# Performance work log

Measured on AMD Instinct MI355X. Metric: run time of the kernel, lower is better.

Reference implementation:

```python
import jax, jax.numpy as jnp
import numpy as np

B, N, D, H, W = 2, 6, 120, 32, 88
C = 128
Z, HO, WO = 1, 128, 128  # bev_feat_shape
N_POINTS = 1_000_000


def setup_inputs() -> dict:
    key = jax.random.key(0)
    k1, k2, k3, k4, k5 = jax.random.split(key, 5)
    depth = jax.random.normal(k1, (B, N, D, H, W), dtype=jnp.float32)
    feat = jax.random.normal(k2, (B, N, C, H, W), dtype=jnp.float32)
    ranks_depth = jax.random.randint(k3, (N_POINTS,), 0, B * N * D * H * W, dtype=jnp.int32)
    ranks_feat = jax.random.randint(k4, (N_POINTS,), 0, B * N * H * W, dtype=jnp.int32)
    ranks_bev = jnp.sort(jax.random.randint(k5, (N_POINTS,), 0, B * Z * HO * WO, dtype=jnp.int32))
    # Derive intervals (consecutive runs of equal ranks_bev), as the CUDA op expects.
    rb = np.asarray(ranks_bev)
    starts = np.concatenate([[0], np.nonzero(np.diff(rb))[0] + 1]).astype(np.int32)
    lengths = np.diff(np.concatenate([starts, [rb.shape[0]]])).astype(np.int32)
    return {
        "depth": depth,
        "feat": feat,
        "ranks_depth": ranks_depth,
        "ranks_feat": ranks_feat,
        "ranks_bev": ranks_bev,
        "interval_starts": jnp.asarray(starts),
        "interval_lengths": jnp.asarray(lengths),
    }


def reference(depth, feat, ranks_depth, ranks_feat, ranks_bev, interval_starts, interval_lengths):
    b, n, c, h, w = feat.shape
    # feat laid out [b,n,c,h,w]; ranks_feat indexes (b,n,h,w) positions -> put c last.
    feat_flat = feat.transpose(0, 1, 3, 4, 2).reshape(-1, c)  # [b*n*h*w, c]
    depth_flat = depth.reshape(-1)                            # [b*n*d*h*w]
    # Gather depth scalar and feature row per point, multiply.
    prod = depth_flat[ranks_depth][:, None] * feat_flat[ranks_feat]  # [n_points, c]
    # Interval-based accumulation == segment-sum over sorted ranks_bev.
    num_cells = b * Z * HO * WO
    out = jax.ops.segment_sum(prod, ranks_bev, num_segments=num_cells)  # [b*z*h*w, c]
    out = out.reshape(b, Z, HO, WO, c).transpose(0, 4, 1, 2, 3)  # [b, c, z, h, w]
    return out
```

## Files before the change

kernel.cpp:

```cpp
#include <hip/hip_runtime.h>
#include <hip/hip_bf16.h>

#define HW_    2816
#define C_     128
#define BN_    12
#define SPAT_  16384
#define CELLS_ 32768
#define CB_    64

#define TF_BX     88
#define TF_BY     4
#define TF_BLOCKS (TF_BX * TF_BY * BN_)
#define PG_BLOCKS 1024
#define IV_BLOCKS 128

__device__ __forceinline__ unsigned int f2bf_rne(float x) {
    const unsigned int u = __float_as_uint(x);
    return (u + 0x7fffu + ((u >> 16) & 1u)) >> 16;
}

__global__ __launch_bounds__(256) void prep_k(
        const float* __restrict__ feat, __hip_bfloat16* __restrict__ featT,
        const float* __restrict__ depth, const int* __restrict__ rd,
        const int* __restrict__ rf, unsigned int* __restrict__ pair, int n_points,
        const int* __restrict__ istart, const int* __restrict__ ilen,
        const int* __restrict__ rb, int4* __restrict__ iv4,
        int* __restrict__ map, int n_intervals) {
    __shared__ float tile[32][33];
    const int bid = blockIdx.x;
    const int tid = threadIdx.x;

    if (bid < TF_BLOCKS) {
        const int bn  = bid / (TF_BX * TF_BY);
        const int r   = bid - bn * (TF_BX * TF_BY);
        const int c0  = (r / TF_BX) * 32;
        const int hw0 = (r - (r / TF_BX) * TF_BX) * 32;
        const int x = tid & 31, y = tid >> 5;
        const float* src = feat + ((size_t)bn * C_ + c0) * HW_ + hw0;
        #pragma unroll
        for (int yy = y; yy < 32; yy += 8)
            tile[yy][x] = src[(size_t)yy * HW_ + x];
        __syncthreads();
        __hip_bfloat16* dst = featT + ((size_t)bn * HW_ + hw0) * C_ + c0;
        #pragma unroll
        for (int yy = y; yy < 32; yy += 8)
            dst[(size_t)yy * C_ + x] = __float2bfloat16(tile[x][yy]);
    } else if (bid < TF_BLOCKS + PG_BLOCKS) {
        const int t = (bid - TF_BLOCKS) * 256 + tid;
        const int stride = PG_BLOCKS * 256;
        for (int base = t; base < n_points; base += 4 * stride) {
            int ii[4], idx[4], rfv[4];
            float v[4];
            #pragma unroll
            for (int u = 0; u < 4; ++u) {
                ii[u] = base + u * stride;
                const int cl = ii[u] < n_points ? ii[u] : base;
                idx[u] = rd[cl];
                rfv[u] = rf[cl];
            }
            #pragma unroll
            for (int u = 0; u < 4; ++u) v[u] = depth[idx[u]];
            #pragma unroll
            for (int u = 0; u < 4; ++u)
                if (ii[u] < n_points)
                    pair[ii[u]] = (f2bf_rne(v[u]) << 16) | (unsigned)rfv[u];
        }
    } else {
        const int ivl = (bid - TF_BLOCKS - PG_BLOCKS) * 256 + tid;
        if (ivl < n_intervals) {
            const int s = istart[ivl];
            const int c = rb[s];
            iv4[ivl] = make_int4(s, ilen[ivl], c, 0);
            map[c] = ivl;
            const int cnext = (ivl + 1 < n_intervals) ? rb[istart[ivl + 1]] : CELLS_;
            for (int cc = c + 1; cc < cnext; ++cc) map[cc] = -1;
            if (ivl == 0) for (int cc = 0; cc < c; ++cc) map[cc] = -1;
        }
    }
}

__global__ __launch_bounds__(1024, 4) void bevpool_cells_k(
        const unsigned int* __restrict__ pair,
        const uint4* __restrict__ featT,
        const int4* __restrict__ iv4,
        const int* __restrict__ map,
        float* __restrict__ out) {
    __shared__ float lds[CB_][68];
    const int half  = blockIdx.x & 1;
    const int cb    = blockIdx.x >> 1;
    const int cell0 = cb * CB_;
    const int tid   = threadIdx.x;

    #pragma unroll
    for (int i = tid; i < CB_ * 68; i += 1024) (&lds[0][0])[i] = 0.f;
    __syncthreads();

    const int widx = tid >> 6;
    const int lane = tid & 63;
    const int grp  = lane >> 3;
    const int sl   = lane & 7;
    const size_t hoff = (size_t)(half * 8 + sl);
    const int cl0  = widx * 4;

    const int4 m4 = *(const int4*)&map[cell0 + cl0];
    const int m[4] = {m4.x, m4.y, m4.z, m4.w};
    int4 vq[4];
    #pragma unroll
    for (int q = 0; q < 4; ++q) vq[q] = iv4[m[q] < 0 ? 0 : m[q]];

    #pragma unroll
    for (int q = 0; q < 4; ++q) {
        if (m[q] < 0) continue;
        const int start = vq[q].x;
        const int end   = vq[q].x + vq[q].y;

        float acc[8] = {0.f, 0.f, 0.f, 0.f, 0.f, 0.f, 0.f, 0.f};
        for (int i = start + grp; i < end; i += 32) {
            int cl_[4];
            unsigned pr_[4];
            float d_[4];
            uint4 f_[4];
            #pragma unroll
            for (int u = 0; u < 4; ++u) {
                const int ii = i + 8 * u;
                cl_[u] = (ii < end) ? ii : i;
            }
            #pragma unroll
            for (int u = 0; u < 4; ++u) pr_[u] = pair[cl_[u]];
            #pragma unroll
            for (int u = 0; u < 4; ++u) d_[u] = __uint_as_float(pr_[u] & 0xffff0000u);
            #pragma unroll
            for (int u = 1; u < 4; ++u) d_[u] = (i + 8 * u < end) ? d_[u] : 0.f;
            #pragma unroll
            for (int u = 0; u < 4; ++u)
                f_[u] = featT[(size_t)(pr_[u] & 0xffffu) * 16 + hoff];
            #pragma unroll
            for (int u = 0; u < 4; ++u) {
                const float d = d_[u];
                acc[0] = fmaf(d, __uint_as_float(f_[u].x << 16),         acc[0]);
                acc[1] = fmaf(d, __uint_as_float(f_[u].x & 0xffff0000u), acc[1]);
                acc[2] = fmaf(d, __uint_as_float(f_[u].y << 16),         acc[2]);
                acc[3] = fmaf(d, __uint_as_float(f_[u].y & 0xffff0000u), acc[3]);
                acc[4] = fmaf(d, __uint_as_float(f_[u].z << 16),         acc[4]);
                acc[5] = fmaf(d, __uint_as_float(f_[u].z & 0xffff0000u), acc[5]);
                acc[6] = fmaf(d, __uint_as_float(f_[u].w << 16),         acc[6]);
                acc[7] = fmaf(d, __uint_as_float(f_[u].w & 0xffff0000u), acc[7]);
            }
        }
        #pragma unroll
        for (int c = 0; c < 8; ++c) {
            acc[c] += __shfl_down(acc[c], 32);
            acc[c] += __shfl_down(acc[c], 16);
            acc[c] += __shfl_down(acc[c], 8);
        }
        if (grp == 0) {
            #pragma unroll
            for (int c = 0; c < 8; ++c) lds[cl0 + q][sl * 8 + c] = acc[c];
        }
    }
    __syncthreads();

    const int cl  = tid & 63;
    const int chb = tid >> 6;
    const int b   = cell0 >> 14;
    const int sp0 = cell0 & (SPAT_ - 1);
    float* obase = out + ((size_t)b * C_ + half * 64) * SPAT_ + sp0;
    #pragma unroll
    for (int it = 0; it < 4; ++it) {
        const int ch = chb + 16 * it;
        obase[(size_t)ch * SPAT_ + cl] = lds[cl][ch];
    }
}

__global__ __launch_bounds__(256) void bevpool_fallback_k(const float* __restrict__ depth,
                                                          const float* __restrict__ feat,
                                                          const int* __restrict__ rd_arr,
                                                          const int* __restrict__ rf_arr,
                                                          const int* __restrict__ rb,
                                                          const int* __restrict__ istart,
                                                          const int* __restrict__ ilen,
                                                          float* __restrict__ out,
                                                          int n_intervals) {
    const int wave = (int)((blockIdx.x * blockDim.x + threadIdx.x) >> 6);
    const int lane = threadIdx.x & 63;
    if (wave >= n_intervals) return;
    const int start = istart[wave];
    const int len   = ilen[wave];
    const int cell  = rb[start];
    float ax = 0.f, ay = 0.f;
    const int end = start + len;
    for (int i = start; i < end; ++i) {
        const int rfi = rf_arr[i];
        const int bn  = rfi / HW_;
        const int hw  = rfi - bn * HW_;
        const float d = depth[rd_arr[i]];
        const float* frow = feat + (size_t)bn * (C_ * HW_) + hw;
        ax = fmaf(d, frow[(size_t)(2 * lane)     * HW_], ax);
        ay = fmaf(d, frow[(size_t)(2 * lane + 1) * HW_], ay);
    }
    const int b  = cell >> 14;
    const int sp = cell & (SPAT_ - 1);
    float* o = out + (size_t)b * ((size_t)C_ * SPAT_) + sp;
    o[(size_t)(2 * lane)     * SPAT_] = ax;
    o[(size_t)(2 * lane + 1) * SPAT_] = ay;
}

extern "C" void kernel_launch(void* const* d_in, const int* in_sizes, int n_in,
                              void* d_out, int out_size, void* d_ws, size_t ws_size,
                              hipStream_t stream) {
    const float* depth  = (const float*)d_in[0];
    const float* feat   = (const float*)d_in[1];
    const int*   rd     = (const int*)d_in[2];
    const int*   rf     = (const int*)d_in[3];
    const int*   rb     = (const int*)d_in[4];
    const int*   istart = (const int*)d_in[5];
    const int*   ilen   = (const int*)d_in[6];
    float*       out    = (float*)d_out;
    const int n_intervals = in_sizes[5];
    const int n_points    = in_sizes[2];

    const size_t featT_bytes = (size_t)BN_ * HW_ * C_ * sizeof(__hip_bfloat16);
    const size_t pair_bytes  = ((size_t)n_points * sizeof(unsigned int) + 15) & ~(size_t)15;
    const size_t iv4_bytes   = (size_t)CELLS_ * sizeof(int4);
    const size_t map_bytes   = (size_t)CELLS_ * sizeof(int);

    if (ws_size >= featT_bytes + pair_bytes + iv4_bytes + map_bytes &&
        n_intervals <= CELLS_) {
        __hip_bfloat16* featT = (__hip_bfloat16*)d_ws;
        unsigned int*   pair  = (unsigned int*)((char*)d_ws + featT_bytes);
        int4*           iv4   = (int4*)((char*)d_ws + featT_bytes + pair_bytes);
        int*            map   = (int*)((char*)d_ws + featT_bytes + pair_bytes + iv4_bytes);

        const int prep_blocks = TF_BLOCKS + PG_BLOCKS + IV_BLOCKS;
        prep_k<<<prep_blocks, 256, 0, stream>>>(
            feat, featT, depth, rd, rf, pair, n_points,
            istart, ilen, rb, iv4, map, n_intervals);

        bevpool_cells_k<<<(CELLS_ / CB_) * 2, 1024, 0, stream>>>(
            pair, (const uint4*)featT, iv4, map, out);
    } else {
        hipMemsetAsync(out, 0, (size_t)out_size * sizeof(float), stream);
        const int blocks = (n_intervals + 3) / 4;
        bevpool_fallback_k<<<blocks, 256, 0, stream>>>(
            depth, feat, rd, rf, rb, istart, ilen, out, n_intervals);
    }
}
```

Before: 59.03 us.

## Remap bevpool work: one 4-lane group per cell across quarter channel splits

The accumulation kernel now gives each BEV cell to a 4-lane group that walks the cell's points sequentially, instead of spreading one cell over a whole 64-lane wave. The cross-lane shuffle reduction goes away. Channels are split into four 32-channel quarters across blocks, with 128 cells per 512-thread block. This cuts idle lanes and reduction overhead for cells that hold only a few points (around 30 on average), but point lists are read four times and load imbalance between cells grows. The prep kernel's gather loop is also changed to a fixed 8-way unroll with half the blocks, which assumes 512*256*8 covers n_points.

```diff
diff --git a/kernel.cpp b/kernel.cpp
--- a/kernel.cpp
+++ b/kernel.cpp
@@ -6,12 +6,12 @@
 #define BN_    12
 #define SPAT_  16384
 #define CELLS_ 32768
-#define CB_    64
+#define CPB_   128
 
 #define TF_BX     88
 #define TF_BY     4
 #define TF_BLOCKS (TF_BX * TF_BY * BN_)
-#define PG_BLOCKS 1024
+#define PG_BLOCKS 512
 #define IV_BLOCKS 128
 
 __device__ __forceinline__ unsigned int f2bf_rne(float x) {
@@ -47,23 +47,23 @@
             dst[(size_t)yy * C_ + x] = __float2bfloat16(tile[x][yy]);
     } else if (bid < TF_BLOCKS + PG_BLOCKS) {
         const int t = (bid - TF_BLOCKS) * 256 + tid;
-        const int stride = PG_BLOCKS * 256;
-        for (int base = t; base < n_points; base += 4 * stride) {
-            int ii[4], idx[4], rfv[4];
-            float v[4];
-            #pragma unroll
-            for (int u = 0; u < 4; ++u) {
-                ii[u] = base + u * stride;
-                const int cl = ii[u] < n_points ? ii[u] : base;
-                idx[u] = rd[cl];
-                rfv[u] = rf[cl];
-            }
-            #pragma unroll
-            for (int u = 0; u < 4; ++u) v[u] = depth[idx[u]];
-            #pragma unroll
-            for (int u = 0; u < 4; ++u)
-                if (ii[u] < n_points)
-                    pair[ii[u]] = (f2bf_rne(v[u]) << 16) | (unsigned)rfv[u];
+        const int S = PG_BLOCKS * 256;
+        int idx[8], rfv[8];
+        float v[8];
+        #pragma unroll
+        for (int u = 0; u < 8; ++u) {
+            const int ii = t + u * S;
+            const int cl = ii < n_points ? ii : t;
+            idx[u] = rd[cl];
+            rfv[u] = rf[cl];
+        }
+        #pragma unroll
+        for (int u = 0; u < 8; ++u) v[u] = depth[idx[u]];
+        #pragma unroll
+        for (int u = 0; u < 8; ++u) {
+            const int ii = t + u * S;
+            if (ii < n_points)
+                pair[ii] = (f2bf_rne(v[u]) << 16) | (unsigned)rfv[u];
         }
     } else {
         const int ivl = (bid - TF_BLOCKS - PG_BLOCKS) * 256 + tid;
@@ -79,50 +79,44 @@
     }
 }
 
-__global__ __launch_bounds__(1024, 4) void bevpool_cells_k(
+__global__ __launch_bounds__(512, 4) void bevpool_cells_k(
         const unsigned int* __restrict__ pair,
         const uint4* __restrict__ featT,
         const int4* __restrict__ iv4,
         const int* __restrict__ map,
         float* __restrict__ out) {
-    __shared__ float lds[CB_][68];
-    const int half  = blockIdx.x & 1;
-    const int cb    = blockIdx.x >> 1;
-    const int cell0 = cb * CB_;
+    __shared__ float lds[CPB_][36];
+    const int q     = blockIdx.x & 3;
+    const int cb    = blockIdx.x >> 2;
+    const int cell0 = cb * CPB_;
     const int tid   = threadIdx.x;
 
-    #pragma unroll
-    for (int i = tid; i < CB_ * 68; i += 1024) (&lds[0][0])[i] = 0.f;
+    for (int i = tid; i < CPB_ * 36; i += 512) (&lds[0][0])[i] = 0.f;
     __syncthreads();
 
-    const int widx = tid >> 6;
+    const int w    = tid >> 6;
     const int lane = tid & 63;
-    const int grp  = lane >> 3;
-    const int sl   = lane & 7;
-    const size_t hoff = (size_t)(half * 8 + sl);
-    const int cl0  = widx * 4;
-
-    const int4 m4 = *(const int4*)&map[cell0 + cl0];
-    const int m[4] = {m4.x, m4.y, m4.z, m4.w};
-    int4 vq[4];
-    #pragma unroll
-    for (int q = 0; q < 4; ++q) vq[q] = iv4[m[q] < 0 ? 0 : m[q]];
-
-    #pragma unroll
-    for (int q = 0; q < 4; ++q) {
-        if (m[q] < 0) continue;
-        const int start = vq[q].x;
-        const int end   = vq[q].x + vq[q].y;
-
+    const int g    = lane >> 2;
+    const int sl   = lane & 3;
+    const int lc   = w * 16 + g;
+    const size_t hoff = (size_t)(q * 4 + sl);
+
+    const int m  = map[cell0 + lc];
+    const int4 v = iv4[m < 0 ? 0 : m];
+
+    if (m >= 0) {
+        const int start = v.x;
+        const int end   = v.x + v.y;
         float acc[8] = {0.f, 0.f, 0.f, 0.f, 0.f, 0.f, 0.f, 0.f};
-        for (int i = start + grp; i < end; i += 32) {
+
+        for (int i = start; i < end; i += 4) {
             int cl_[4];
             unsigned pr_[4];
             float d_[4];
             uint4 f_[4];
             #pragma unroll
             for (int u = 0; u < 4; ++u) {
-                const int ii = i + 8 * u;
+                const int ii = i + u;
                 cl_[u] = (ii < end) ? ii : i;
             }
             #pragma unroll
@@ -130,7 +124,7 @@
             #pragma unroll
             for (int u = 0; u < 4; ++u) d_[u] = __uint_as_float(pr_[u] & 0xffff0000u);
             #pragma unroll
-            for (int u = 1; u < 4; ++u) d_[u] = (i + 8 * u < end) ? d_[u] : 0.f;
+            for (int u = 1; u < 4; ++u) d_[u] = (i + u < end) ? d_[u] : 0.f;
             #pragma unroll
             for (int u = 0; u < 4; ++u)
                 f_[u] = featT[(size_t)(pr_[u] & 0xffffu) * 16 + hoff];
@@ -148,26 +142,18 @@
             }
         }
         #pragma unroll
-        for (int c = 0; c < 8; ++c) {
-            acc[c] += __shfl_down(acc[c], 32);
-            acc[c] += __shfl_down(acc[c], 16);
-            acc[c] += __shfl_down(acc[c], 8);
-        }
-        if (grp == 0) {
-            #pragma unroll
-            for (int c = 0; c < 8; ++c) lds[cl0 + q][sl * 8 + c] = acc[c];
-        }
+        for (int c = 0; c < 8; ++c) lds[lc][sl * 8 + c] = acc[c];
     }
     __syncthreads();
 
-    const int cl  = tid & 63;
-    const int chb = tid >> 6;
+    const int cl  = tid & 127;
+    const int chb = tid >> 7;
     const int b   = cell0 >> 14;
     const int sp0 = cell0 & (SPAT_ - 1);
-    float* obase = out + ((size_t)b * C_ + half * 64) * SPAT_ + sp0;
+    float* obase = out + ((size_t)b * C_ + q * 32) * SPAT_ + sp0;
     #pragma unroll
-    for (int it = 0; it < 4; ++it) {
-        const int ch = chb + 16 * it;
+    for (int it = 0; it < 8; ++it) {
+        const int ch = chb + 4 * it;
         obase[(size_t)ch * SPAT_ + cl] = lds[cl][ch];
     }
 }
@@ -236,7 +222,7 @@
             feat, featT, depth, rd, rf, pair, n_points,
             istart, ilen, rb, iv4, map, n_intervals);
 
-        bevpool_cells_k<<<(CELLS_ / CB_) * 2, 1024, 0, stream>>>(
+        bevpool_cells_k<<<(CELLS_ / CPB_) * 4, 512, 0, stream>>>(
             pair, (const uint4*)featT, iv4, map, out);
     } else {
         hipMemsetAsync(out, 0, (size_t)out_size * sizeof(float), stream);
```

New measurement: 72.53 us. 22.9% more time.

## Software-pipeline pair loads across cells and raise occupancy in bevpool kernel

Applied to the files above, without the earlier changes.

The cell-accumulation kernel now prefetches the first batch of pair entries for the next cells before it processes the current one. This overlaps the dependent pair-to-featT gather latency across the four cells each wave handles. The launch bound rises to 8 blocks per CU, and LDS padding shrinks from 68 to 65 columns. The prep kernel's point-gather section is also changed to half as many blocks, each with a single unrolled 8-way batch and no grid-stride loop. The extra prefetch registers could fight with the higher occupancy target. The single-batch gather depends on n_points fitting in 512*256*8 entries.

```diff
diff --git a/kernel.cpp b/kernel.cpp
--- a/kernel.cpp
+++ b/kernel.cpp
@@ -11,7 +11,7 @@
 #define TF_BX     88
 #define TF_BY     4
 #define TF_BLOCKS (TF_BX * TF_BY * BN_)
-#define PG_BLOCKS 1024
+#define PG_BLOCKS 512
 #define IV_BLOCKS 128
 
 __device__ __forceinline__ unsigned int f2bf_rne(float x) {
@@ -47,23 +47,23 @@
             dst[(size_t)yy * C_ + x] = __float2bfloat16(tile[x][yy]);
     } else if (bid < TF_BLOCKS + PG_BLOCKS) {
         const int t = (bid - TF_BLOCKS) * 256 + tid;
-        const int stride = PG_BLOCKS * 256;
-        for (int base = t; base < n_points; base += 4 * stride) {
-            int ii[4], idx[4], rfv[4];
-            float v[4];
-            #pragma unroll
-            for (int u = 0; u < 4; ++u) {
-                ii[u] = base + u * stride;
-                const int cl = ii[u] < n_points ? ii[u] : base;
-                idx[u] = rd[cl];
-                rfv[u] = rf[cl];
-            }
-            #pragma unroll
-            for (int u = 0; u < 4; ++u) v[u] = depth[idx[u]];
-            #pragma unroll
-            for (int u = 0; u < 4; ++u)
-                if (ii[u] < n_points)
-                    pair[ii[u]] = (f2bf_rne(v[u]) << 16) | (unsigned)rfv[u];
+        const int S = PG_BLOCKS * 256;
+        int idx[8], rfv[8];
+        float v[8];
+        #pragma unroll
+        for (int u = 0; u < 8; ++u) {
+            const int ii = t + u * S;
+            const int cl = ii < n_points ? ii : t;
+            idx[u] = rd[cl];
+            rfv[u] = rf[cl];
+        }
+        #pragma unroll
+        for (int u = 0; u < 8; ++u) v[u] = depth[idx[u]];
+        #pragma unroll
+        for (int u = 0; u < 8; ++u) {
+            const int ii = t + u * S;
+            if (ii < n_points)
+                pair[ii] = (f2bf_rne(v[u]) << 16) | (unsigned)rfv[u];
         }
     } else {
         const int ivl = (bid - TF_BLOCKS - PG_BLOCKS) * 256 + tid;
@@ -79,20 +79,67 @@
     }
 }
 
-__global__ __launch_bounds__(1024, 4) void bevpool_cells_k(
+#define FMA8(d, f)                                                   \
+    acc[0] = fmaf(d, __uint_as_float((f).x << 16),         acc[0]);  \
+    acc[1] = fmaf(d, __uint_as_float((f).x & 0xffff0000u), acc[1]);  \
+    acc[2] = fmaf(d, __uint_as_float((f).y << 16),         acc[2]);  \
+    acc[3] = fmaf(d, __uint_as_float((f).y & 0xffff0000u), acc[3]);  \
+    acc[4] = fmaf(d, __uint_as_float((f).z << 16),         acc[4]);  \
+    acc[5] = fmaf(d, __uint_as_float((f).z & 0xffff0000u), acc[5]);  \
+    acc[6] = fmaf(d, __uint_as_float((f).w << 16),         acc[6]);  \
+    acc[7] = fmaf(d, __uint_as_float((f).w & 0xffff0000u), acc[7]);
+
+__device__ __forceinline__ void cell_finish(
+        const float d_[4], const uint4 f_[4], int i0, int e,
+        const unsigned int* __restrict__ pair,
+        const uint4* __restrict__ featT, size_t hoff,
+        int grp, int sl, float* __restrict__ lds_row) {
+    float acc[8] = {0.f, 0.f, 0.f, 0.f, 0.f, 0.f, 0.f, 0.f};
+    #pragma unroll
+    for (int u = 0; u < 4; ++u) { FMA8(d_[u], f_[u]); }
+    for (int i = i0 + 32; i < e; i += 32) {
+        unsigned pr2[4];
+        float d2[4];
+        uint4 f2[4];
+        #pragma unroll
+        for (int u = 0; u < 4; ++u) {
+            const int ii = i + 8 * u;
+            pr2[u] = pair[(ii < e) ? ii : i];
+        }
+        #pragma unroll
+        for (int u = 0; u < 4; ++u) d2[u] = __uint_as_float(pr2[u] & 0xffff0000u);
+        #pragma unroll
+        for (int u = 1; u < 4; ++u) d2[u] = (i + 8 * u < e) ? d2[u] : 0.f;
+        #pragma unroll
+        for (int u = 0; u < 4; ++u) f2[u] = featT[(size_t)(pr2[u] & 0xffffu) * 16 + hoff];
+        #pragma unroll
+        for (int u = 0; u < 4; ++u) { FMA8(d2[u], f2[u]); }
+    }
+    #pragma unroll
+    for (int c = 0; c < 8; ++c) {
+        acc[c] += __shfl_down(acc[c], 32);
+        acc[c] += __shfl_down(acc[c], 16);
+        acc[c] += __shfl_down(acc[c], 8);
+    }
+    if (grp == 0) {
+        #pragma unroll
+        for (int c = 0; c < 8; ++c) lds_row[sl * 8 + c] = acc[c];
+    }
+}
+
+__global__ __launch_bounds__(1024, 8) void bevpool_cells_k(
         const unsigned int* __restrict__ pair,
         const uint4* __restrict__ featT,
         const int4* __restrict__ iv4,
         const int* __restrict__ map,
         float* __restrict__ out) {
-    __shared__ float lds[CB_][68];
+    __shared__ float lds[CB_][65];
     const int half  = blockIdx.x & 1;
     const int cb    = blockIdx.x >> 1;
     const int cell0 = cb * CB_;
     const int tid   = threadIdx.x;
 
-    #pragma unroll
-    for (int i = tid; i < CB_ * 68; i += 1024) (&lds[0][0])[i] = 0.f;
+    for (int i = tid; i < CB_ * 65; i += 1024) (&lds[0][0])[i] = 0.f;
     __syncthreads();
 
     const int widx = tid >> 6;
@@ -104,60 +151,57 @@
 
     const int4 m4 = *(const int4*)&map[cell0 + cl0];
     const int m[4] = {m4.x, m4.y, m4.z, m4.w};
-    int4 vq[4];
-    #pragma unroll
-    for (int q = 0; q < 4; ++q) vq[q] = iv4[m[q] < 0 ? 0 : m[q]];
-
-    #pragma unroll
-    for (int q = 0; q < 4; ++q) {
-        if (m[q] < 0) continue;
-        const int start = vq[q].x;
-        const int end   = vq[q].x + vq[q].y;
-
-        float acc[8] = {0.f, 0.f, 0.f, 0.f, 0.f, 0.f, 0.f, 0.f};
-        for (int i = start + grp; i < end; i += 32) {
-            int cl_[4];
-            unsigned pr_[4];
-            float d_[4];
-            uint4 f_[4];
-            #pragma unroll
-            for (int u = 0; u < 4; ++u) {
-                const int ii = i + 8 * u;
-                cl_[u] = (ii < end) ? ii : i;
-            }
-            #pragma unroll
-            for (int u = 0; u < 4; ++u) pr_[u] = pair[cl_[u]];
-            #pragma unroll
-            for (int u = 0; u < 4; ++u) d_[u] = __uint_as_float(pr_[u] & 0xffff0000u);
-            #pragma unroll
-            for (int u = 1; u < 4; ++u) d_[u] = (i + 8 * u < end) ? d_[u] : 0.f;
-            #pragma unroll
-            for (int u = 0; u < 4; ++u)
-                f_[u] = featT[(size_t)(pr_[u] & 0xffffu) * 16 + hoff];
-            #pragma unroll
-            for (int u = 0; u < 4; ++u) {
-                const float d = d_[u];
-                acc[0] = fmaf(d, __uint_as_float(f_[u].x << 16),         acc[0]);
-                acc[1] = fmaf(d, __uint_as_float(f_[u].x & 0xffff0000u), acc[1]);
-                acc[2] = fmaf(d, __uint_as_float(f_[u].y << 16),         acc[2]);
-                acc[3] = fmaf(d, __uint_as_float(f_[u].y & 0xffff0000u), acc[3]);
-                acc[4] = fmaf(d, __uint_as_float(f_[u].z << 16),         acc[4]);
-                acc[5] = fmaf(d, __uint_as_float(f_[u].z & 0xffff0000u), acc[5]);
-                acc[6] = fmaf(d, __uint_as_float(f_[u].w << 16),         acc[6]);
-                acc[7] = fmaf(d, __uint_as_float(f_[u].w & 0xffff0000u), acc[7]);
-            }
-        }
-        #pragma unroll
-        for (int c = 0; c < 8; ++c) {
-            acc[c] += __shfl_down(acc[c], 32);
-            acc[c] += __shfl_down(acc[c], 16);
-            acc[c] += __shfl_down(acc[c], 8);
-        }
-        if (grp == 0) {
-            #pragma unroll
-            for (int c = 0; c < 8; ++c) lds[cl0 + q][sl * 8 + c] = acc[c];
-        }
-    }
+    int s[4], e[4];
+    {
+        const int4 v0 = iv4[m[0] < 0 ? 0 : m[0]];
+        const int4 v1 = iv4[m[1] < 0 ? 0 : m[1]];
+        const int4 v2 = iv4[m[2] < 0 ? 0 : m[2]];
+        const int4 v3 = iv4[m[3] < 0 ? 0 : m[3]];
+        s[0] = v0.x; e[0] = v0.x + v0.y;
+        s[1] = v1.x; e[1] = v1.x + v1.y;
+        s[2] = v2.x; e[2] = v2.x + v2.y;
+        s[3] = v3.x; e[3] = v3.x + v3.y;
+    }
+
+#define PF(dst, qq)                                         \
+    {                                                       \
+        const int i0_ = s[qq] + grp;                        \
+        _Pragma("unroll")                                   \
+        for (int u = 0; u < 4; ++u) {                       \
+            const int ii = i0_ + 8 * u;                     \
+            dst[u] = pair[(ii < e[qq]) ? ii : s[qq]];       \
+        }                                                   \
+    }
+
+#define CELL(qq, PR, PFNEXT)                                                  \
+    {                                                                         \
+        const int i0_ = s[qq] + grp;                                          \
+        uint4 f_[4];                                                          \
+        _Pragma("unroll")                                                     \
+        for (int u = 0; u < 4; ++u)                                           \
+            f_[u] = featT[(size_t)(PR[u] & 0xffffu) * 16 + hoff];             \
+        float d_[4];                                                          \
+        _Pragma("unroll")                                                     \
+        for (int u = 0; u < 4; ++u) {                                         \
+            const float dv = __uint_as_float(PR[u] & 0xffff0000u);            \
+            d_[u] = (i0_ + 8 * u < e[qq]) ? dv : 0.f;                         \
+        }                                                                     \
+        PFNEXT                               \
+        if (m[qq] >= 0)                                                       \
+            cell_finish(d_, f_, i0_, e[qq], pair, featT, hoff,                \
+                        grp, sl, &lds[cl0 + qq][0]);                          \
+    }
+
+    unsigned prA[4], prB[4];
+    PF(prA, 0)
+    PF(prB, 1)
+    CELL(0, prA, PF(prA, 2))
+    CELL(1, prB, PF(prB, 3))
+    CELL(2, prA, )
+    CELL(3, prB, )
+#undef CELL
+#undef PF
+
     __syncthreads();
 
     const int cl  = tid & 63;
```

Result: slower. 64.05 us (+8.5%).
